# Kernel optimization log

Measured on AMD Instinct MI355X. Metric: run time of the kernel, lower is better.

The kernel has to match this reference:

```python
import jax, jax.numpy as jnp
import numpy as np

EPSILON = 1e-8
K = 3
PAD = K // 2


def setup_inputs() -> dict:
    key = jax.random.key(0)
    k1, k2, k3, k4 = jax.random.split(key, 4)
    B, FI, FO, H, W, DSTYLE = 8, 512, 512, 64, 64, 512
    return {
        "x": jax.random.normal(k1, (B, FI, H, W), dtype=jnp.float32),
        "style": jax.random.normal(k2, (B, DSTYLE), dtype=jnp.float32),
        "w": jax.random.normal(k3, (FO, FI, K, K), dtype=jnp.float32),
        "fc_w": jax.random.normal(k4, (FI, DSTYLE), dtype=jnp.float32),  # modLinear weight [dim_out=fi, dim_in=dim_style]
        "fc_b": jnp.zeros((FI,), dtype=jnp.float32),
    }


def reference(x, style, w, fc_w, fc_b):
    B, FI, H, W = x.shape
    FO = w.shape[0]
    DSTYLE = fc_w.shape[1]
    fc_scale = DSTYLE ** (-0.5)            # modLinear w_scale (lr_mult=1)
    w_scale = (FI * K * K) ** (-0.5)       # modConv w_scale

    # modLinear: style -> per-input-channel modulation s, shape [B, FI]
    s = style @ (fc_w * fc_scale).T + fc_b

    # Demod factor: d[b, fo] = rsqrt(sum_{fi,k,k} (w_scale * w * s[b,fi])^2 + eps)
    wsq = jnp.sum((w * w_scale) ** 2, axis=(2, 3))          # [FO, FI]
    d = jax.lax.rsqrt(jnp.einsum('of,bf->bo', wsq, s ** 2) + EPSILON)  # [B, FO]

    # Equivalent to per-sample grouped conv: scale input channels by s,
    # conv with shared base weight, scale output channels by demod.
    xm = x * s[:, :, None, None]
    y = jax.lax.conv_general_dilated(
        xm, w * w_scale,
        window_strides=(1, 1),
        padding=((PAD, PAD), (PAD, PAD)),
        dimension_numbers=('NCHW', 'OIHW', 'NCHW'),
    )
    return y * d[:, :, None, None]
```

## Files before the change

### kernel.cpp

```cpp
#include <hip/hip_runtime.h>


typedef __bf16 bf16_t;
typedef __bf16 bf16x8 __attribute__((ext_vector_type(8)));
typedef float floatx4 __attribute__((ext_vector_type(4)));

#define HW_ 4096
#define FCSCALE 0.04419417382415922f
#define WSCALE  0.014731391274719742f

__device__ __forceinline__ void gload_lds16(const bf16_t* g, bf16_t* l) {
  __builtin_amdgcn_global_load_lds(
      (const __attribute__((address_space(1))) void*)g,
      (__attribute__((address_space(3))) void*)l, 16, 0, 0);
}

__global__ void k_style(const float* __restrict__ style, const float* __restrict__ fc_w,
                        const float* __restrict__ fc_b, float* __restrict__ s_out) {
  int o = blockIdx.x * 4 + (threadIdx.x >> 6);
  int lane = threadIdx.x & 63;
  int b = o >> 9, fi = o & 511;
  const float4* st = (const float4*)(style + b * 512);
  const float4* fw = (const float4*)(fc_w + (size_t)fi * 512);
  float4 a0 = st[lane * 2],     w0 = fw[lane * 2];
  float4 a1 = st[lane * 2 + 1], w1 = fw[lane * 2 + 1];
  float acc = a0.x * w0.x + a0.y * w0.y + a0.z * w0.z + a0.w * w0.w
            + a1.x * w1.x + a1.y * w1.y + a1.z * w1.z + a1.w * w1.w;
#pragma unroll
  for (int d = 32; d >= 1; d >>= 1) acc += __shfl_xor(acc, d, 64);
  if (lane == 0) s_out[o] = acc * FCSCALE + fc_b[fi];
}

__global__ void k_wsq_wt(const float* __restrict__ w, float* __restrict__ wsq,
                         bf16_t* __restrict__ wt) {
  int idx = blockIdx.x * 256 + threadIdx.x;
  int fo = idx >> 9, fi = idx & 511;
  const float* wp = w + (size_t)idx * 9;
  float v[9], q = 0.f;
#pragma unroll
  for (int k = 0; k < 9; ++k) { v[k] = wp[k] * WSCALE; q += v[k] * v[k]; }
  wsq[idx] = q;
#pragma unroll
  for (int k = 0; k < 9; ++k)
    wt[((((size_t)k * 64) + (fi >> 3)) * 512 + fo) * 8 + (fi & 7)] = (bf16_t)v[k];
}

__global__ void k_demod(const float* __restrict__ wsq, const float* __restrict__ s,
                        float* __restrict__ dcoef) {
  int o = blockIdx.x * 4 + (threadIdx.x >> 6);
  int lane = threadIdx.x & 63;
  int b = o >> 9, fo = o & 511;
  const float4* wq = (const float4*)(wsq + (size_t)fo * 512);
  const float4* sp = (const float4*)(s + b * 512);
  float acc = 0.f;
#pragma unroll
  for (int i = 0; i < 2; ++i) {
    float4 q = wq[lane * 2 + i], sv = sp[lane * 2 + i];
    acc += q.x * sv.x * sv.x + q.y * sv.y * sv.y + q.z * sv.z * sv.z + q.w * sv.w * sv.w;
  }
#pragma unroll
  for (int d = 32; d >= 1; d >>= 1) acc += __shfl_xor(acc, d, 64);
  if (lane == 0) dcoef[o] = rsqrtf(acc + 1e-8f);
}

__global__ void k_modx(const float* __restrict__ x, const float* __restrict__ s,
                       bf16_t* __restrict__ xT) {
  __shared__ float tile[32][65];
  int b = blockIdx.z;
  int fi0 = blockIdx.x * 32;
  int h = blockIdx.y;
  int t = threadIdx.x;
  int c4 = (t & 15) * 4, fr = t >> 4;
#pragma unroll
  for (int i = 0; i < 2; ++i) {
    int fi_l = i * 16 + fr;
    float sv = s[b * 512 + fi0 + fi_l];
    float4 v = *(const float4*)(x + ((size_t)(b * 512 + fi0 + fi_l)) * HW_ + h * 64 + c4);
    tile[fi_l][c4] = v.x * sv; tile[fi_l][c4 + 1] = v.y * sv;
    tile[fi_l][c4 + 2] = v.z * sv; tile[fi_l][c4 + 3] = v.w * sv;
  }
  __syncthreads();
  int g_l = t >> 6, wcol = t & 63;
  bf16x8 vv;
#pragma unroll
  for (int j = 0; j < 8; ++j) vv[j] = (bf16_t)tile[g_l * 8 + j][wcol];
  *(bf16x8*)&xT[((((size_t)(b * 64 + h)) * 64 + (fi0 >> 3) + g_l) * 64 + wcol) * 8] = vv;
}

__global__ __launch_bounds__(256, 2) void k_conv(const bf16_t* __restrict__ wt,
                                                 const bf16_t* __restrict__ xT,
                                                 const float* __restrict__ dcoef,
                                                 const bf16_t* __restrict__ zerobuf,
                                                 float* __restrict__ out) {
  __shared__ __align__(16) bf16_t xls[3][4 * 256 * 8];
  __shared__ __align__(16) bf16_t wls[3][4 * 128 * 8];

  int b   = blockIdx.x;
  int foB = blockIdx.y;
  int hq  = blockIdx.z;
  int t = threadIdx.x;
  int wv = t >> 6, lane = t & 63, quad = lane >> 4, l16 = lane & 15;
  int h0 = hq * 4;
  int fo_l = t & 127, chunk_hi = t >> 7;

  const bf16_t* xTb = xT + (size_t)b * 64 * 64 * 64 * 8;

  floatx4 acc[8][4];
#pragma unroll
  for (int i = 0; i < 8; ++i)
#pragma unroll
    for (int j = 0; j < 4; ++j) acc[i][j] = (floatx4){0.f, 0.f, 0.f, 0.f};

  auto stage = [&](int it, int pf) {
    int tap = it >> 4;
    int g0 = (it & 15) * 4;
    int kh = tap / 3, kw = tap - kh * 3;
    int rg = h0 + wv + kh - 1;
    int cg = lane + kw - 1;
    bool valid = ((unsigned)rg < 64u) && ((unsigned)cg < 64u);
#pragma unroll
    for (int itw = 0; itw < 2; ++itw) {
      int cw = itw * 2 + chunk_hi;
      gload_lds16(wt + ((((size_t)tap * 64) + g0 + cw) * 512 + foB * 128 + fo_l) * 8,
                  &wls[pf][(itw * 256 + wv * 64) * 8]);
    }
#pragma unroll
    for (int it4 = 0; it4 < 4; ++it4) {
      const bf16_t* src = valid
          ? xTb + (((size_t)rg * 64 + g0 + it4) * 64 + cg) * 8
          : zerobuf;
      gload_lds16(src, &xls[pf][(it4 * 256 + wv * 64) * 8]);
    }
  };

  auto compute = [&](int pc) {
    bf16x8 bfr[4];
#pragma unroll
    for (int j = 0; j < 4; ++j)
      bfr[j] = *(const bf16x8*)&xls[pc][(quad * 256 + wv * 64 + j * 16 + l16) * 8];
    __builtin_amdgcn_s_setprio(1);
#pragma unroll
    for (int i = 0; i < 8; ++i) {
      bf16x8 afr = *(const bf16x8*)&wls[pc][(quad * 128 + i * 16 + l16) * 8];
#pragma unroll
      for (int j = 0; j < 4; ++j)
        acc[i][j] = __builtin_amdgcn_mfma_f32_16x16x32_bf16(afr, bfr[j], acc[i][j], 0, 0, 0);
    }
    __builtin_amdgcn_s_setprio(0);
  };

  stage(0, 0);
  stage(1, 1);

  int p = 0, pn = 2;
  for (int it = 0; it < 142; ++it) {
    stage(it + 2, pn);
    asm volatile("s_waitcnt vmcnt(12)" ::: "memory");
    __builtin_amdgcn_s_barrier();
    __builtin_amdgcn_sched_barrier(0);
    compute(p);
    asm volatile("s_waitcnt lgkmcnt(0)" ::: "memory");
    __builtin_amdgcn_s_barrier();
    __builtin_amdgcn_sched_barrier(0);
    p = (p == 2) ? 0 : p + 1;
    pn = (pn == 2) ? 0 : pn + 1;
  }
  asm volatile("s_waitcnt vmcnt(6)" ::: "memory");
  __builtin_amdgcn_s_barrier();
  __builtin_amdgcn_sched_barrier(0);
  compute(p);
  p = (p == 2) ? 0 : p + 1;
  asm volatile("s_waitcnt vmcnt(0)" ::: "memory");
  __builtin_amdgcn_s_barrier();
  __builtin_amdgcn_sched_barrier(0);
  compute(p);

  int h = h0 + wv;
#pragma unroll
  for (int i = 0; i < 8; ++i) {
#pragma unroll
    for (int rr = 0; rr < 4; ++rr) {
      int fo_g = foB * 128 + i * 16 + quad * 4 + rr;
      float dm = dcoef[b * 512 + fo_g];
      float* op = out + ((size_t)((b * 512 + fo_g) * 64 + h)) * 64;
#pragma unroll
      for (int j = 0; j < 4; ++j)
        op[j * 16 + l16] = acc[i][j][rr] * dm;
    }
  }
}

extern "C" void kernel_launch(void* const* d_in, const int* in_sizes, int n_in,
                              void* d_out, int out_size, void* d_ws, size_t ws_size,
                              hipStream_t stream) {
  const float* x     = (const float*)d_in[0];
  const float* style = (const float*)d_in[1];
  const float* w     = (const float*)d_in[2];
  const float* fc_w  = (const float*)d_in[3];
  const float* fc_b  = (const float*)d_in[4];
  float* out = (float*)d_out;
  char* ws = (char*)d_ws;

  float*  s       = (float*)(ws);
  float*  dcoef   = (float*)(ws + 16384);
  float*  wsq     = (float*)(ws + 32768);
  bf16_t* zerobuf = (bf16_t*)(ws + 1081344);
  bf16_t* wt      = (bf16_t*)(ws + 1081600);
  bf16_t* xT      = (bf16_t*)(ws + 5800192);

  hipMemsetAsync(zerobuf, 0, 256, stream);
  k_style<<<1024, 256, 0, stream>>>(style, fc_w, fc_b, s);
  k_wsq_wt<<<1024, 256, 0, stream>>>(w, wsq, wt);
  k_demod<<<1024, 256, 0, stream>>>(wsq, s, dcoef);
  k_modx<<<dim3(16, 64, 8), 256, 0, stream>>>(x, s, xT);
  k_conv<<<dim3(8, 4, 16), 256, 0, stream>>>(wt, xT, dcoef, zerobuf, out);
}
```

Measured before the change: 271.1 us.

## Load conv input fragments directly to registers, keep weights in 4-stage LDS ring

```diff
diff --git a/kernel.cpp b/kernel.cpp
--- a/kernel.cpp
+++ b/kernel.cpp
@@ -8,6 +8,8 @@
 #define HW_ 4096
 #define FCSCALE 0.04419417382415922f
 #define WSCALE  0.014731391274719742f
+
+#define VMCNT(n) asm volatile("s_waitcnt vmcnt(" #n ")" ::: "memory")
 
 __device__ __forceinline__ void gload_lds16(const bf16_t* g, bf16_t* l) {
   __builtin_amdgcn_global_load_lds(
@@ -92,8 +94,7 @@
                                                  const float* __restrict__ dcoef,
                                                  const bf16_t* __restrict__ zerobuf,
                                                  float* __restrict__ out) {
-  __shared__ __align__(16) bf16_t xls[3][4 * 256 * 8];
-  __shared__ __align__(16) bf16_t wls[3][4 * 128 * 8];
+  __shared__ __align__(16) bf16_t wls[4 * 4 * 128 * 8];
 
   int b   = blockIdx.x;
   int foB = blockIdx.y;
@@ -111,69 +112,87 @@
 #pragma unroll
     for (int j = 0; j < 4; ++j) acc[i][j] = (floatx4){0.f, 0.f, 0.f, 0.f};
 
-  auto stage = [&](int it, int pf) {
+  auto stage_w = [&](int it, int pf) {
+    int tap = it >> 4;
+    int g0 = (it & 15) * 4;
+#pragma unroll
+    for (int itw = 0; itw < 2; ++itw) {
+      int cw = itw * 2 + chunk_hi;
+      gload_lds16(wt + ((((size_t)tap * 64) + g0 + cw) * 512 + foB * 128 + fo_l) * 8,
+                  &wls[(size_t)pf * 4096 + (itw * 256 + wv * 64) * 8]);
+    }
+  };
+
+  auto load_x = [&](int it, bf16x8* xf) {
     int tap = it >> 4;
     int g0 = (it & 15) * 4;
     int kh = tap / 3, kw = tap - kh * 3;
     int rg = h0 + wv + kh - 1;
-    int cg = lane + kw - 1;
-    bool valid = ((unsigned)rg < 64u) && ((unsigned)cg < 64u);
-#pragma unroll
-    for (int itw = 0; itw < 2; ++itw) {
-      int cw = itw * 2 + chunk_hi;
-      gload_lds16(wt + ((((size_t)tap * 64) + g0 + cw) * 512 + foB * 128 + fo_l) * 8,
-                  &wls[pf][(itw * 256 + wv * 64) * 8]);
-    }
-#pragma unroll
-    for (int it4 = 0; it4 < 4; ++it4) {
-      const bf16_t* src = valid
-          ? xTb + (((size_t)rg * 64 + g0 + it4) * 64 + cg) * 8
-          : zerobuf;
-      gload_lds16(src, &xls[pf][(it4 * 256 + wv * 64) * 8]);
+    bool rok = (unsigned)rg < 64u;
+    const bf16_t* rowp = xTb + (((size_t)rg * 64 + g0 + quad) * 64) * 8;
+#pragma unroll
+    for (int j = 0; j < 4; ++j) {
+      int c = j * 16 + l16 + kw - 1;
+      const bf16_t* src = (rok && (unsigned)c < 64u) ? rowp + (size_t)c * 8
+                                                     : zerobuf;
+      xf[j] = *(const bf16x8*)src;
     }
   };
 
-  auto compute = [&](int pc) {
-    bf16x8 bfr[4];
-#pragma unroll
-    for (int j = 0; j < 4; ++j)
-      bfr[j] = *(const bf16x8*)&xls[pc][(quad * 256 + wv * 64 + j * 16 + l16) * 8];
+  auto compute = [&](int pc, const bf16x8* xf) {
+    const bf16_t* wb = &wls[(size_t)pc * 4096];
     __builtin_amdgcn_s_setprio(1);
 #pragma unroll
     for (int i = 0; i < 8; ++i) {
-      bf16x8 afr = *(const bf16x8*)&wls[pc][(quad * 128 + i * 16 + l16) * 8];
+      bf16x8 afr = *(const bf16x8*)&wb[(quad * 128 + i * 16 + l16) * 8];
 #pragma unroll
       for (int j = 0; j < 4; ++j)
-        acc[i][j] = __builtin_amdgcn_mfma_f32_16x16x32_bf16(afr, bfr[j], acc[i][j], 0, 0, 0);
+        acc[i][j] = __builtin_amdgcn_mfma_f32_16x16x32_bf16(afr, xf[j], acc[i][j], 0, 0, 0);
     }
     __builtin_amdgcn_s_setprio(0);
   };
 
-  stage(0, 0);
-  stage(1, 1);
-
-  int p = 0, pn = 2;
-  for (int it = 0; it < 142; ++it) {
-    stage(it + 2, pn);
-    asm volatile("s_waitcnt vmcnt(12)" ::: "memory");
+  bf16x8 xfA[4], xfB[4];
+
+  stage_w(0, 0);
+  load_x(0, xfA);
+  stage_w(1, 1);
+
+  for (int it = 0; it < 140; it += 2) {
+    load_x(it + 1, xfB);
+    stage_w(it + 2, (it + 2) & 3);
+    VMCNT(8);
     __builtin_amdgcn_s_barrier();
     __builtin_amdgcn_sched_barrier(0);
-    compute(p);
-    asm volatile("s_waitcnt lgkmcnt(0)" ::: "memory");
+    compute(it & 3, xfA);
+    load_x(it + 2, xfA);
+    stage_w(it + 3, (it + 3) & 3);
+    VMCNT(8);
     __builtin_amdgcn_s_barrier();
     __builtin_amdgcn_sched_barrier(0);
-    p = (p == 2) ? 0 : p + 1;
-    pn = (pn == 2) ? 0 : pn + 1;
-  }
-  asm volatile("s_waitcnt vmcnt(6)" ::: "memory");
-  __builtin_amdgcn_s_barrier();
-  __builtin_amdgcn_sched_barrier(0);
-  compute(p);
-  p = (p == 2) ? 0 : p + 1;
-  asm volatile("s_waitcnt vmcnt(0)" ::: "memory");
-  __builtin_amdgcn_s_barrier();
-  __builtin_amdgcn_sched_barrier(0);
-  compute(p);
+    compute((it + 1) & 3, xfB);
+  }
+  load_x(141, xfB);
+  stage_w(142, 2);
+  VMCNT(8);
+  __builtin_amdgcn_s_barrier();
+  __builtin_amdgcn_sched_barrier(0);
+  compute(0, xfA);
+  load_x(142, xfA);
+  stage_w(143, 3);
+  VMCNT(8);
+  __builtin_amdgcn_s_barrier();
+  __builtin_amdgcn_sched_barrier(0);
+  compute(1, xfB);
+  load_x(143, xfB);
+  VMCNT(6);
+  __builtin_amdgcn_s_barrier();
+  __builtin_amdgcn_sched_barrier(0);
+  compute(2, xfA);
+  VMCNT(0);
+  __builtin_amdgcn_s_barrier();
+  __builtin_amdgcn_sched_barrier(0);
+  compute(3, xfB);
 
   int h = h0 + wv;
 #pragma unroll
```

Result: slower. 277.9 us (+2.5%).
